# Performance work log

Measured on AMD Instinct MI355X. Metric: run time of the kernel, lower is better.

## Reference

```python
import jax, jax.numpy as jnp
import numpy as np

H = 768
NH = 12
HD = 64
FF = 3072
EPS = 1e-12


def layer_norm(x, g, b):
    mu = jnp.mean(x, axis=-1, keepdims=True)
    var = jnp.mean((x - mu) ** 2, axis=-1, keepdims=True)
    return (x - mu) * jax.lax.rsqrt(var + EPS) * g + b


def setup_inputs() -> dict:
    key = jax.random.key(0)
    ks = jax.random.split(key, 16)
    B, S, L = 16, 512, 50
    s = 0.02
    return {
        "hidden_states": jax.random.normal(ks[0], (B, S, H), jnp.float32),
        "attention_mask": jnp.zeros((B, 1, 1, S), jnp.float32),
        "past_key": jax.random.normal(ks[1], (B, NH, L, HD), jnp.float32),
        "past_value": jax.random.normal(ks[2], (B, NH, L, HD), jnp.float32),
        "Wq": jax.random.normal(ks[3], (H, H), jnp.float32) * s,
        "bq": jnp.zeros((H,), jnp.float32),
        "Wk": jax.random.normal(ks[4], (H, H), jnp.float32) * s,
        "bk": jnp.zeros((H,), jnp.float32),
        "Wv": jax.random.normal(ks[5], (H, H), jnp.float32) * s,
        "bv": jnp.zeros((H,), jnp.float32),
        "Wo": jax.random.normal(ks[6], (H, H), jnp.float32) * s,
        "bo": jnp.zeros((H,), jnp.float32),
        "ln1_g": jnp.ones((H,), jnp.float32),
        "ln1_b": jnp.zeros((H,), jnp.float32),
        "Wi": jax.random.normal(ks[7], (H, FF), jnp.float32) * s,
        "bi": jnp.zeros((FF,), jnp.float32),
        "Wf": jax.random.normal(ks[8], (FF, H), jnp.float32) * s,
        "bf": jnp.zeros((H,), jnp.float32),
        "ln2_g": jnp.ones((H,), jnp.float32),
        "ln2_b": jnp.zeros((H,), jnp.float32),
    }


def reference(hidden_states, attention_mask, past_key, past_value,
              Wq, bq, Wk, bk, Wv, bv, Wo, bo, ln1_g, ln1_b,
              Wi, bi, Wf, bf, ln2_g, ln2_b):
    B, S, _ = hidden_states.shape
    L = past_key.shape[2]

    def heads(x):  # [B,S,H] -> [B,NH,S,HD]
        return x.reshape(B, S, NH, HD).transpose(0, 2, 1, 3)

    q = heads(hidden_states @ Wq + bq)
    k = heads(hidden_states @ Wk + bk)
    v = heads(hidden_states @ Wv + bv)

    # faithful to source bug: past_key_values[0] concatenated into BOTH k and v
    k = jnp.concatenate([past_key, k], axis=2)  # [B,NH,L+S,HD]
    v = jnp.concatenate([past_key, v], axis=2)

    scores = jnp.einsum('bhqd,bhkd->bhqk', q, k) / jnp.sqrt(jnp.float32(HD))
    # visual mask positions get +1.0 (torch.ones), faithful to source
    vis_mask = jnp.ones((B, 1, 1, L), scores.dtype)
    full_mask = jnp.concatenate([vis_mask, attention_mask], axis=-1)
    scores = scores + full_mask

    probs = jax.nn.softmax(scores, axis=-1)
    ctx = jnp.einsum('bhqk,bhkd->bhqd', probs, v)  # [B,NH,S,HD]
    ctx = ctx.transpose(0, 2, 1, 3).reshape(B, S, H)

    attn_out = layer_norm(ctx @ Wo + bo + hidden_states, ln1_g, ln1_b)

    inter = jax.nn.gelu(attn_out @ Wi + bi, approximate=False)
    layer_out = layer_norm(inter @ Wf + bf + attn_out, ln2_g, ln2_b)
    return layer_out
```

## Files before the change

### kernel.cpp

```cpp
#include <hip/hip_runtime.h>
#include <math.h>

#define HDIM 64
#define NHEAD 12
#define HDN 768
#define QKVN 2304
#define FFDIM 3072
#define LPAST 50
#define SEQ 512
#define NBATCH 16
#define TKV (LPAST + SEQ)
#define TKVP 576
#define MTOK (NBATCH * SEQ)
#define NBH (NBATCH * NHEAD)

typedef __attribute__((ext_vector_type(8))) short short8;
typedef __attribute__((ext_vector_type(4))) float f32x4;

__device__ __forceinline__ ushort f2bf(float x) {
    union { float f; unsigned u; } c; c.f = x;
    unsigned r = (c.u + 0x7fffu + ((c.u >> 16) & 1u)) >> 16;
    return (ushort)r;
}
__device__ __forceinline__ float bf2f(ushort u) { return __uint_as_float((unsigned)u << 16); }
__device__ __forceinline__ float geluf(float v) {
    return 0.5f * v * (1.0f + erff(v * 0.70710678118654752f));
}

#define GLOAD_LDS16(gsrc, ldst)                                                    \
    __builtin_amdgcn_global_load_lds(                                              \
        (const __attribute__((address_space(1))) void*)(gsrc),                     \
        (__attribute__((address_space(3))) void*)(ldst), 16, 0, 0)

__global__ __launch_bounds__(256) void cast_bf(const float* __restrict__ x,
                                               ushort* __restrict__ y, int n4) {
    int i = blockIdx.x * 256 + threadIdx.x;
    if (i >= n4) return;
    float4 v = ((const float4*)x)[i];
    ushort4 o; o.x = f2bf(v.x); o.y = f2bf(v.y); o.z = f2bf(v.z); o.w = f2bf(v.w);
    ((ushort4*)y)[i] = o;
}

__global__ __launch_bounds__(256) void pack_bias(const float* __restrict__ bq,
                                                 const float* __restrict__ bk,
                                                 const float* __restrict__ bv,
                                                 float* __restrict__ o) {
    int i = blockIdx.x * 256 + threadIdx.x;
    if (i >= QKVN) return;
    o[i] = i < HDN ? bq[i] : (i < 2 * HDN ? bk[i - HDN] : bv[i - 2 * HDN]);
}

__global__ __launch_bounds__(256) void transpose_cast(const float* __restrict__ W,
                                                      ushort* __restrict__ WT,
                                                      int K, int N) {
    __shared__ float t[32][33];
    const int n0 = blockIdx.x * 32, k0 = blockIdx.y * 32;
    const int tx = threadIdx.x & 31, ty = threadIdx.x >> 5;
    #pragma unroll
    for (int i = 0; i < 4; ++i)
        t[ty + i * 8][tx] = W[(size_t)(k0 + ty + i * 8) * N + n0 + tx];
    __syncthreads();
    #pragma unroll
    for (int i = 0; i < 4; ++i)
        WT[(size_t)(n0 + ty + i * 8) * K + k0 + tx] = f2bf(t[tx][ty + i * 8]);
}

__global__ __launch_bounds__(256) void transpose_cast4(
    const float* __restrict__ W0, const float* __restrict__ W1,
    const float* __restrict__ W2, const float* __restrict__ W3,
    ushort* __restrict__ T0, ushort* __restrict__ T1,
    ushort* __restrict__ T2, ushort* __restrict__ T3) {
    __shared__ float t[32][33];
    const int z = blockIdx.z;
    const float* W = z == 0 ? W0 : z == 1 ? W1 : z == 2 ? W2 : W3;
    ushort* WT = z == 0 ? T0 : z == 1 ? T1 : z == 2 ? T2 : T3;
    const int n0 = blockIdx.x * 32, k0 = blockIdx.y * 32;
    const int tx = threadIdx.x & 31, ty = threadIdx.x >> 5;
    #pragma unroll
    for (int i = 0; i < 4; ++i)
        t[ty + i * 8][tx] = W[(size_t)(k0 + ty + i * 8) * HDN + n0 + tx];
    __syncthreads();
    #pragma unroll
    for (int i = 0; i < 4; ++i)
        WT[(size_t)(n0 + ty + i * 8) * HDN + k0 + tx] = f2bf(t[tx][ty + i * 8]);
}

template<int EPI>
__global__ __launch_bounds__(256) void gemm_mfma3(
    const ushort* __restrict__ A, const ushort* __restrict__ B,
    int lda, int ldb,
    const float* __restrict__ bias, const float* __restrict__ resid,
    const ushort* __restrict__ resid_bf,
    void* __restrict__ Cout, int M, int N, int K)
{
    __shared__ ushort sm[3 * 8192];

    const int tid = threadIdx.x;
    const int lane = tid & 63;
    const int wv = tid >> 6;
    const int wr = wv >> 1, wc = wv & 1;
    const int bm = blockIdx.x * 128, bn = blockIdx.y * 128;
    const int lr = lane & 15, lg = lane >> 4;
    const int swzu = ((lr * 64 + lg * 16) ^ ((lr & 8) << 2)) >> 1;

    int srow[2], skk[2];
    #pragma unroll
    for (int r = 0; r < 2; ++r) {
        int o = (tid + 256 * r) * 16;
        int st = o >> 10;
        int q = o & 1023;
        q ^= ((q >> 9) & 1) << 5;
        srow[r] = st * 16 + (q >> 6);
        skk[r] = (q & 63) >> 1;
    }
    const ushort* Abase = A + (size_t)bm * lda;
    const ushort* Bbase = B + (size_t)bn * ldb;
    const int nt = K >> 5;

    f32x4 acc[4][4] = {};

#define STAGE(T, BUF)                                                            \
    do {                                                                         \
        const int k0_ = (T) << 5;                                                \
        ushort* base_ = sm + (BUF) * 8192;                                       \
        _Pragma("unroll")                                                        \
        for (int r_ = 0; r_ < 2; ++r_) {                                         \
            int sl_ = tid + 256 * r_;                                            \
            GLOAD_LDS16(Abase + (size_t)srow[r_] * lda + k0_ + skk[r_],          \
                        (char*)base_ + sl_ * 16);                                \
        }                                                                        \
        _Pragma("unroll")                                                        \
        for (int r_ = 0; r_ < 2; ++r_) {                                         \
            int sl_ = tid + 256 * r_;                                            \
            GLOAD_LDS16(Bbase + (size_t)srow[r_] * ldb + k0_ + skk[r_],          \
                        (char*)(base_ + 4096) + sl_ * 16);                       \
        }                                                                        \
    } while (0)

    STAGE(0, 0);
    STAGE(1, 1);
    asm volatile("s_waitcnt vmcnt(4)" ::: "memory");
    __builtin_amdgcn_sched_barrier(0);
    __builtin_amdgcn_s_barrier();
    __builtin_amdgcn_sched_barrier(0);

    int buf = 0;
    for (int t = 0; t < nt; ++t) {
        if (t + 2 < nt) {
            int nbuf = buf + 2; if (nbuf >= 3) nbuf -= 3;
            STAGE(t + 2, nbuf);
        }
        const ushort* ab = sm + buf * 8192;
        short8 af[4], bfv[4];
        #pragma unroll
        for (int i = 0; i < 4; ++i) {
            af[i]  = *(const short8*)(ab + (wr * 4 + i) * 512 + swzu);
            bfv[i] = *(const short8*)(ab + 4096 + (wc * 4 + i) * 512 + swzu);
        }
        __builtin_amdgcn_s_setprio(1);
        #pragma unroll
        for (int i = 0; i < 4; ++i)
            #pragma unroll
            for (int j = 0; j < 4; ++j)
                acc[i][j] = __builtin_amdgcn_mfma_f32_16x16x32_bf16(
                    af[i], bfv[j], acc[i][j], 0, 0, 0);
        __builtin_amdgcn_s_setprio(0);
        if (t + 2 < nt)
            asm volatile("s_waitcnt vmcnt(4)" ::: "memory");
        else
            asm volatile("s_waitcnt vmcnt(0)" ::: "memory");
        __builtin_amdgcn_sched_barrier(0);
        __builtin_amdgcn_s_barrier();
        __builtin_amdgcn_sched_barrier(0);
        buf = buf + 1 == 3 ? 0 : buf + 1;
    }
#undef STAGE

    #pragma unroll
    for (int i = 0; i < 4; ++i) {
        #pragma unroll
        for (int j = 0; j < 4; ++j) {
            const int col = bn + wc * 64 + j * 16 + lr;
            const float bv = bias[col];
            #pragma unroll
            for (int rr = 0; rr < 4; ++rr) {
                const int row = bm + wr * 64 + i * 16 + (lane >> 4) * 4 + rr;
                const size_t idx = (size_t)row * N + col;
                float v = acc[i][j][rr] + bv;
                if (EPI == 0) {
                    ((ushort*)Cout)[idx] = f2bf(v);
                } else if (EPI == 1) {
                    ((float*)Cout)[idx] = v + resid[idx];
                } else if (EPI == 2) {
                    ((ushort*)Cout)[idx] = f2bf(geluf(v));
                } else {
                    ((float*)Cout)[idx] = v + bf2f(resid_bf[idx]);
                }
            }
        }
    }
}

__global__ __launch_bounds__(256) void kvK(
    const ushort* __restrict__ qkv, const float* __restrict__ past_key,
    ushort* __restrict__ kf)
{
    const size_t total = (size_t)NBH * TKV * HDIM;
    size_t idx = (size_t)blockIdx.x * 256 + threadIdx.x;
    if (idx >= total) return;
    int d = idx & 63;
    size_t r = idx >> 6;
    int t = (int)(r % TKV);
    int bh = (int)(r / TKV);
    ushort kv_;
    if (t < LPAST) {
        kv_ = f2bf(past_key[((size_t)bh * LPAST + t) * HDIM + d]);
    } else {
        int b = bh / NHEAD, h = bh % NHEAD;
        kv_ = qkv[((size_t)(b * SEQ + (t - LPAST))) * QKVN + HDN + h * HDIM + d];
    }
    kf[idx] = kv_;
}

__global__ __launch_bounds__(256) void kvVT(
    const ushort* __restrict__ qkv, const float* __restrict__ past_key,
    ushort* __restrict__ vt)
{
    __shared__ ushort td[64][72];
    const int bh = blockIdx.x / 9;
    const int t0 = (blockIdx.x % 9) * 64;
    const int b = bh / NHEAD, h = bh % NHEAD;
    const int trow = threadIdx.x >> 2, seg = threadIdx.x & 3;
    const int t = t0 + trow;

    ushort vals[16];
    if (t < LPAST) {
        const float* pk = past_key + ((size_t)bh * LPAST + t) * HDIM + seg * 16;
        #pragma unroll
        for (int i = 0; i < 4; ++i) {
            float4 f = ((const float4*)pk)[i];
            vals[i * 4 + 0] = f2bf(f.x); vals[i * 4 + 1] = f2bf(f.y);
            vals[i * 4 + 2] = f2bf(f.z); vals[i * 4 + 3] = f2bf(f.w);
        }
    } else if (t < TKV) {
        const ushort* vp = qkv + ((size_t)(b * SEQ + (t - LPAST))) * QKVN
                               + 2 * HDN + h * HDIM + seg * 16;
        uint4 u0 = ((const uint4*)vp)[0], u1 = ((const uint4*)vp)[1];
        *(uint4*)&vals[0] = u0; *(uint4*)&vals[8] = u1;
    } else {
        #pragma unroll
        for (int i = 0; i < 16; ++i) vals[i] = 0;
    }
    #pragma unroll
    for (int i = 0; i < 16; ++i) td[trow][seg * 16 + i] = vals[i];
    __syncthreads();

    const int d = threadIdx.x >> 2;
    ushort o[16];
    #pragma unroll
    for (int i = 0; i < 16; ++i) o[i] = td[seg * 16 + i][d];
    ushort* dst = vt + ((size_t)bh * HDIM + d) * TKVP + t0 + seg * 16;
    *(uint4*)dst = *(uint4*)&o[0];
    *(uint4*)(dst + 8) = *(uint4*)&o[8];
}

__global__ __launch_bounds__(256) void attn3(
    const ushort* __restrict__ qkv, const ushort* __restrict__ kf,
    const ushort* __restrict__ vt, const float* __restrict__ mask,
    ushort* __restrict__ ctx)
{
    __shared__ ushort Ks[64 * 64];
    __shared__ ushort Vs[64 * 64];
    __shared__ ushort Ps[4][16 * 64];

    const int wv = threadIdx.x >> 6, lane = threadIdx.x & 63;
    const int lr = lane & 15, lg = lane >> 4;
    const int bid = blockIdx.x;
    const int xcd = bid & 7, gi = bid >> 3;
    const int bh = xcd * (NBH / 8) + (gi >> 3);
    const int s0 = (gi & 7) * 64;
    const int b = bh / NHEAD, h = bh % NHEAD;

    short8 af[2];
    {
        const ushort* qp = qkv + ((size_t)(b * SEQ + s0 + wv * 16 + lr)) * QKVN
                               + h * HDIM + lg * 8;
        af[0] = *(const short8*)qp;
        af[1] = *(const short8*)(qp + 32);
    }

    const ushort* kbase = kf + (size_t)bh * TKV * HDIM;
    const ushort* vbase = vt + (size_t)bh * HDIM * TKVP;

    float m[4] = {-1e30f, -1e30f, -1e30f, -1e30f};
    float l[4] = {};
    f32x4 ctxa[4] = {};

    for (int kt = 0; kt < 9; ++kt) {
        const int t0 = kt * 64;
        #pragma unroll
        for (int r = 0; r < 2; ++r) {
            int sl = (int)threadIdx.x + 256 * r;
            int row = sl >> 3, p = sl & 7;
            int j = p ^ (row & 7);
            int trow = t0 + row; if (trow > TKV - 1) trow = TKV - 1;
            GLOAD_LDS16(kbase + ((size_t)trow << 6) + j * 8, (char*)Ks + sl * 16);
        }
        #pragma unroll
        for (int r = 0; r < 2; ++r) {
            int sl = (int)threadIdx.x + 256 * r;
            int row = sl >> 3, p = sl & 7;
            int j = p ^ (row & 7);
            GLOAD_LDS16(vbase + (size_t)row * TKVP + t0 + j * 8, (char*)Vs + sl * 16);
        }
        __syncthreads();

        f32x4 sa[4] = {};
        #pragma unroll
        for (int kb = 0; kb < 4; ++kb) {
            const int key = kb * 16 + lr;
            #pragma unroll
            for (int c = 0; c < 2; ++c) {
                const int phys = (c * 4 + lg) ^ (key & 7);
                short8 kfrag = *(const short8*)&Ks[key * 64 + phys * 8];
                sa[kb] = __builtin_amdgcn_mfma_f32_16x16x32_bf16(
                    af[c], kfrag, sa[kb], 0, 0, 0);
            }
        }

        float scv[4][4];
        #pragma unroll
        for (int kb = 0; kb < 4; ++kb) {
            const int t = t0 + kb * 16 + lr;
            float add = 0.0f;
            bool dead = (t >= TKV);
            if (!dead) add = (t < LPAST) ? 1.0f : mask[(size_t)b * SEQ + (t - LPAST)];
            #pragma unroll
            for (int r = 0; r < 4; ++r)
                scv[kb][r] = dead ? -1e30f : fmaf(sa[kb][r], 0.125f, add);
        }

        #pragma unroll
        for (int r = 0; r < 4; ++r) {
            float mx = fmaxf(fmaxf(scv[0][r], scv[1][r]), fmaxf(scv[2][r], scv[3][r]));
            mx = fmaxf(mx, __shfl_xor(mx, 1));
            mx = fmaxf(mx, __shfl_xor(mx, 2));
            mx = fmaxf(mx, __shfl_xor(mx, 4));
            mx = fmaxf(mx, __shfl_xor(mx, 8));
            const float mn = fmaxf(m[r], mx);
            const float f = __expf(m[r] - mn);
            m[r] = mn;
            l[r] *= f;
            #pragma unroll
            for (int dg = 0; dg < 4; ++dg) ctxa[dg][r] *= f;
            const int q_ = lg * 4 + r;
            #pragma unroll
            for (int kb = 0; kb < 4; ++kb) {
                float p = __expf(scv[kb][r] - mn);
                l[r] += p;
                const int key = kb * 16 + lr;
                const int phys = (key >> 3) ^ (q_ & 7);
                Ps[wv][q_ * 64 + phys * 8 + (key & 7)] = f2bf(p);
            }
        }

        short8 pa[2];
        #pragma unroll
        for (int c = 0; c < 2; ++c) {
            const int phys = (c * 4 + lg) ^ (lr & 7);
            pa[c] = *(const short8*)&Ps[wv][lr * 64 + phys * 8];
        }
        #pragma unroll
        for (int dg = 0; dg < 4; ++dg) {
            const int d = dg * 16 + lr;
            #pragma unroll
            for (int c = 0; c < 2; ++c) {
                const int phys = (c * 4 + lg) ^ (d & 7);
                short8 vfrag = *(const short8*)&Vs[d * 64 + phys * 8];
                ctxa[dg] = __builtin_amdgcn_mfma_f32_16x16x32_bf16(
                    pa[c], vfrag, ctxa[dg], 0, 0, 0);
            }
        }
        __syncthreads();
    }

    #pragma unroll
    for (int r = 0; r < 4; ++r) {
        float s = l[r];
        s += __shfl_xor(s, 1); s += __shfl_xor(s, 2);
        s += __shfl_xor(s, 4); s += __shfl_xor(s, 8);
        l[r] = 1.0f / s;
    }
    #pragma unroll
    for (int r = 0; r < 4; ++r) {
        const int q_ = s0 + wv * 16 + lg * 4 + r;
        const size_t base = ((size_t)(b * SEQ + q_)) * HDN + h * HDIM;
        #pragma unroll
        for (int dg = 0; dg < 4; ++dg)
            ctx[base + dg * 16 + lr] = f2bf(ctxa[dg][r] * l[r]);
    }
}

__global__ __launch_bounds__(256) void layernorm2(
    const float* __restrict__ x, const float* __restrict__ g,
    const float* __restrict__ b, float* __restrict__ out,
    ushort* __restrict__ out_bf)
{
    const size_t row = blockIdx.x;
    const float* xr = &x[row * HDN];
    const int t = threadIdx.x;

    float v0 = xr[t], v1 = xr[t + 256], v2 = xr[t + 512];

    __shared__ float red[4];
    float s = v0 + v1 + v2;
    #pragma unroll
    for (int off = 32; off > 0; off >>= 1) s += __shfl_xor(s, off);
    if ((t & 63) == 0) red[t >> 6] = s;
    __syncthreads();
    float mean = (red[0] + red[1] + red[2] + red[3]) * (1.0f / 768.0f);

    float d0 = v0 - mean, d1 = v1 - mean, d2 = v2 - mean;
    float vs = d0 * d0 + d1 * d1 + d2 * d2;
    #pragma unroll
    for (int off = 32; off > 0; off >>= 1) vs += __shfl_xor(vs, off);
    __syncthreads();
    if ((t & 63) == 0) red[t >> 6] = vs;
    __syncthreads();
    float var = (red[0] + red[1] + red[2] + red[3]) * (1.0f / 768.0f);
    float rstd = rsqrtf(var + 1e-12f);

    float o0 = d0 * rstd * g[t] + b[t];
    float o1 = d1 * rstd * g[t + 256] + b[t + 256];
    float o2 = d2 * rstd * g[t + 512] + b[t + 512];
    if (out) {
        out[row * HDN + t] = o0;
        out[row * HDN + t + 256] = o1;
        out[row * HDN + t + 512] = o2;
    }
    if (out_bf) {
        out_bf[row * HDN + t] = f2bf(o0);
        out_bf[row * HDN + t + 256] = f2bf(o1);
        out_bf[row * HDN + t + 512] = f2bf(o2);
    }
}

extern "C" void kernel_launch(void* const* d_in, const int* in_sizes, int n_in,
                              void* d_out, int out_size, void* d_ws, size_t ws_size,
                              hipStream_t stream) {
    const float* hs       = (const float*)d_in[0];
    const float* mask     = (const float*)d_in[1];
    const float* past_key = (const float*)d_in[2];
    const float* Wq = (const float*)d_in[4];
    const float* bq = (const float*)d_in[5];
    const float* Wk = (const float*)d_in[6];
    const float* bk = (const float*)d_in[7];
    const float* Wv = (const float*)d_in[8];
    const float* bv = (const float*)d_in[9];
    const float* Wo = (const float*)d_in[10];
    const float* bo = (const float*)d_in[11];
    const float* ln1_g = (const float*)d_in[12];
    const float* ln1_b = (const float*)d_in[13];
    const float* Wi = (const float*)d_in[14];
    const float* bi = (const float*)d_in[15];
    const float* Wf = (const float*)d_in[16];
    const float* bf_ = (const float*)d_in[17];
    const float* ln2_g = (const float*)d_in[18];
    const float* ln2_b = (const float*)d_in[19];
    float* out = (float*)d_out;

    char* w = (char*)d_ws;
    ushort* WqT   = (ushort*)(w + 0);
    ushort* WoT   = (ushort*)(w + 3538944);
    ushort* WiT   = (ushort*)(w + 4718592);
    ushort* WfT   = (ushort*)(w + 9437184);
    float*  bqkv  = (float*)(w + 14155776);
    ushort* hs_bf = (ushort*)(w + 14172160);
    ushort* qkv   = (ushort*)(w + 26755072);
    ushort* kf    = (ushort*)(w + 64503808);
    ushort* vt    = (ushort*)(w + 78315520);
    ushort* ctx_bf = hs_bf;
    float*  tmp   = (float*)(w + 64503808);
    ushort* inter = (ushort*)(w + 14172160);
    ushort* aln_bf = (ushort*)(w + 89669632);
    ushort* WkT = WqT + (size_t)HDN * HDN;
    ushort* WvT = WqT + (size_t)2 * HDN * HDN;

    dim3 b256(256);

    cast_bf<<<dim3((MTOK * HDN / 4 + 255) / 256), b256, 0, stream>>>(hs, hs_bf, MTOK * HDN / 4);
    pack_bias<<<dim3(9), b256, 0, stream>>>(bq, bk, bv, bqkv);
    transpose_cast4<<<dim3(24, 24, 4), b256, 0, stream>>>(Wq, Wk, Wv, Wo, WqT, WkT, WvT, WoT);
    transpose_cast<<<dim3(96, 24), b256, 0, stream>>>(Wi, WiT, HDN, FFDIM);
    transpose_cast<<<dim3(24, 96), b256, 0, stream>>>(Wf, WfT, FFDIM, HDN);

    gemm_mfma3<0><<<dim3(MTOK / 128, QKVN / 128), b256, 0, stream>>>(
        hs_bf, WqT, HDN, HDN, bqkv, nullptr, nullptr, qkv, MTOK, QKVN, HDN);

    {
        size_t ktot = (size_t)NBH * TKV * HDIM;
        kvK<<<dim3((unsigned)((ktot + 255) / 256)), b256, 0, stream>>>(qkv, past_key, kf);
    }
    kvVT<<<dim3(NBH * 9), b256, 0, stream>>>(qkv, past_key, vt);

    attn3<<<dim3(NBH * 8), b256, 0, stream>>>(qkv, kf, vt, mask, ctx_bf);

    gemm_mfma3<1><<<dim3(MTOK / 128, HDN / 128), b256, 0, stream>>>(
        ctx_bf, WoT, HDN, HDN, bo, hs, nullptr, tmp, MTOK, HDN, HDN);
    layernorm2<<<dim3(MTOK), b256, 0, stream>>>(tmp, ln1_g, ln1_b, nullptr, aln_bf);

    gemm_mfma3<2><<<dim3(MTOK / 128, FFDIM / 128), b256, 0, stream>>>(
        aln_bf, WiT, HDN, HDN, bi, nullptr, nullptr, inter, MTOK, FFDIM, HDN);
    gemm_mfma3<4><<<dim3(MTOK / 128, HDN / 128), b256, 0, stream>>>(
        inter, WfT, FFDIM, FFDIM, bf_, nullptr, aln_bf, tmp, MTOK, HDN, FFDIM);

    layernorm2<<<dim3(MTOK), b256, 0, stream>>>(tmp, ln2_g, ln2_b, out, nullptr);
}
```

Baseline: 275.1 us.

## Add 256x256-tile 8-wave GEMM with 128KB LDS for QKV and FFN-up projections

Adds a new bf16 MFMA GEMM kernel that uses 256x256 output tiles, 512 threads (8 waves), double-buffered 128KB dynamic LDS with XOR swizzling, and interleaved LDS reads, global prefetches and MFMA phases with priority hints. It replaces the 128x128 kernel for the QKV projection and the GELU intermediate GEMM. The aim is higher arithmetic intensity and less global/LDS traffic per FLOP. In exchange it runs one block per CU, and the grids shrink to 32x9 and 32x12 blocks, which may underfill a 256-CU device.

```diff
diff --git a/kernel.cpp b/kernel.cpp
--- a/kernel.cpp
+++ b/kernel.cpp
@@ -83,6 +83,166 @@
     #pragma unroll
     for (int i = 0; i < 4; ++i)
         WT[(size_t)(n0 + ty + i * 8) * HDN + k0 + tx] = f2bf(t[tx][ty + i * 8]);
+}
+
+template<int EPI>
+__global__ __launch_bounds__(512, 1) void gemm8(
+    const ushort* __restrict__ A, const ushort* __restrict__ B,
+    int lda, int ldb, const float* __restrict__ bias,
+    ushort* __restrict__ Cout, int M, int N, int K)
+{
+    extern __shared__ ushort sm[];
+
+    const int tid = threadIdx.x;
+    const int lane = tid & 63;
+    const int wv = tid >> 6;
+    const int wm = wv >> 2, wn = wv & 3;
+    const int lr = lane & 15, lg = lane >> 4;
+    const int bm = blockIdx.x * 256, bn = blockIdx.y * 256;
+    const int nt = K >> 6;
+
+    int srow[2], scol[2];
+    #pragma unroll
+    for (int r = 0; r < 2; ++r) {
+        int o = (tid + 512 * r) * 16;
+        int row = o >> 7;
+        int c16 = (o >> 4) & 7;
+        srow[r] = row;
+        scol[r] = (c16 ^ (row & 7)) * 8;
+    }
+
+#define STG8(srcbase, ld, dstb)                                              \
+    _Pragma("unroll")                                                        \
+    for (int r_ = 0; r_ < 2; ++r_)                                           \
+        GLOAD_LDS16((srcbase) + (size_t)srow[r_] * (ld) + scol[r_],          \
+                    (char*)sm + (dstb) + (tid + 512 * r_) * 16);
+
+#define STGB(T)                                                              \
+    do { int bb_ = ((T) & 1) * 65536 + 32768;                                \
+        STG8(B + (size_t)bn * ldb + (size_t)(T) * 64, ldb, bb_);             \
+        STG8(B + (size_t)(bn + 128) * ldb + (size_t)(T) * 64, ldb, bb_ + 16384); } while (0)
+#define STGA(T)                                                              \
+    do { int ab_ = ((T) & 1) * 65536;                                        \
+        STG8(A + (size_t)bm * lda + (size_t)(T) * 64, lda, ab_);             \
+        STG8(A + (size_t)(bm + 128) * lda + (size_t)(T) * 64, lda, ab_ + 16384); } while (0)
+
+    STGB(0); STGA(0);
+    STGB(1); STGA(1);
+    asm volatile("s_waitcnt vmcnt(8)" ::: "memory");
+    __builtin_amdgcn_sched_barrier(0);
+    __builtin_amdgcn_s_barrier();
+    __builtin_amdgcn_sched_barrier(0);
+
+    const int swz0 = (lg * 8) ^ ((lr & 7) << 3);
+    const int swz1 = (32 + lg * 8) ^ ((lr & 7) << 3);
+
+    short8 af[4][2], bq[4][2];
+    f32x4 acc[8][4] = {};
+
+    for (int T = 0; T < nt; ++T) {
+        const ushort* Ab = sm + (T & 1) * 32768 + wm * 8192;
+        const ushort* Bb = sm + (T & 1) * 32768 + 16384 + (wn >> 1) * 8192 + (wn & 1) * 4096;
+
+        #pragma unroll
+        for (int m = 0; m < 4; ++m) {
+            af[m][0] = *(const short8*)(Ab + (m * 16 + lr) * 64 + swz0);
+            af[m][1] = *(const short8*)(Ab + (m * 16 + lr) * 64 + swz1);
+        }
+        #pragma unroll
+        for (int n = 0; n < 2; ++n) {
+            bq[n][0] = *(const short8*)(Bb + (n * 16 + lr) * 64 + swz0);
+            bq[n][1] = *(const short8*)(Bb + (n * 16 + lr) * 64 + swz1);
+        }
+        __builtin_amdgcn_s_barrier();
+        asm volatile("s_waitcnt lgkmcnt(0)" ::: "memory");
+        __builtin_amdgcn_sched_barrier(0);
+        __builtin_amdgcn_s_setprio(1);
+        #pragma unroll
+        for (int m = 0; m < 4; ++m)
+            #pragma unroll
+            for (int n = 0; n < 2; ++n) {
+                acc[m][n] = __builtin_amdgcn_mfma_f32_16x16x32_bf16(af[m][0], bq[n][0], acc[m][n], 0, 0, 0);
+                acc[m][n] = __builtin_amdgcn_mfma_f32_16x16x32_bf16(af[m][1], bq[n][1], acc[m][n], 0, 0, 0);
+            }
+        __builtin_amdgcn_s_setprio(0);
+
+        #pragma unroll
+        for (int n = 2; n < 4; ++n) {
+            bq[n][0] = *(const short8*)(Bb + (n * 16 + lr) * 64 + swz0);
+            bq[n][1] = *(const short8*)(Bb + (n * 16 + lr) * 64 + swz1);
+        }
+        __builtin_amdgcn_s_barrier();
+        asm volatile("s_waitcnt lgkmcnt(0)" ::: "memory");
+        __builtin_amdgcn_sched_barrier(0);
+        __builtin_amdgcn_s_setprio(1);
+        #pragma unroll
+        for (int m = 0; m < 4; ++m)
+            #pragma unroll
+            for (int n = 2; n < 4; ++n) {
+                acc[m][n] = __builtin_amdgcn_mfma_f32_16x16x32_bf16(af[m][0], bq[n][0], acc[m][n], 0, 0, 0);
+                acc[m][n] = __builtin_amdgcn_mfma_f32_16x16x32_bf16(af[m][1], bq[n][1], acc[m][n], 0, 0, 0);
+            }
+        __builtin_amdgcn_s_setprio(0);
+
+        #pragma unroll
+        for (int m = 0; m < 4; ++m) {
+            af[m][0] = *(const short8*)(Ab + ((m + 4) * 16 + lr) * 64 + swz0);
+            af[m][1] = *(const short8*)(Ab + ((m + 4) * 16 + lr) * 64 + swz1);
+        }
+        __builtin_amdgcn_s_barrier();
+        if (T + 2 < nt) { STGB(T + 2); }
+        asm volatile("s_waitcnt lgkmcnt(0)" ::: "memory");
+        __builtin_amdgcn_sched_barrier(0);
+        __builtin_amdgcn_s_setprio(1);
+        #pragma unroll
+        for (int m = 0; m < 4; ++m)
+            #pragma unroll
+            for (int n = 0; n < 2; ++n) {
+                acc[m + 4][n] = __builtin_amdgcn_mfma_f32_16x16x32_bf16(af[m][0], bq[n][0], acc[m + 4][n], 0, 0, 0);
+                acc[m + 4][n] = __builtin_amdgcn_mfma_f32_16x16x32_bf16(af[m][1], bq[n][1], acc[m + 4][n], 0, 0, 0);
+            }
+        __builtin_amdgcn_s_setprio(0);
+
+        __builtin_amdgcn_s_barrier();
+        if (T + 2 < nt) { STGA(T + 2); }
+        __builtin_amdgcn_sched_barrier(0);
+        __builtin_amdgcn_s_setprio(1);
+        #pragma unroll
+        for (int m = 0; m < 4; ++m)
+            #pragma unroll
+            for (int n = 2; n < 4; ++n) {
+                acc[m + 4][n] = __builtin_amdgcn_mfma_f32_16x16x32_bf16(af[m][0], bq[n][0], acc[m + 4][n], 0, 0, 0);
+                acc[m + 4][n] = __builtin_amdgcn_mfma_f32_16x16x32_bf16(af[m][1], bq[n][1], acc[m + 4][n], 0, 0, 0);
+            }
+        __builtin_amdgcn_s_setprio(0);
+
+        if (T < nt - 1) {
+            if (T + 2 < nt) asm volatile("s_waitcnt vmcnt(8)" ::: "memory");
+            else            asm volatile("s_waitcnt vmcnt(0)" ::: "memory");
+            __builtin_amdgcn_sched_barrier(0);
+            __builtin_amdgcn_s_barrier();
+            __builtin_amdgcn_sched_barrier(0);
+        }
+    }
+#undef STGA
+#undef STGB
+#undef STG8
+
+    #pragma unroll
+    for (int m = 0; m < 8; ++m) {
+        #pragma unroll
+        for (int n = 0; n < 4; ++n) {
+            const int col = bn + wn * 64 + n * 16 + lr;
+            const float bv = bias[col];
+            #pragma unroll
+            for (int rr = 0; rr < 4; ++rr) {
+                const int row = bm + wm * 128 + m * 16 + lg * 4 + rr;
+                const size_t idx = (size_t)row * N + col;
+                float v = acc[m][n][rr] + bv;
+                Cout[idx] = f2bf(EPI == 2 ? geluf(v) : v);
+            }
+        }
+    }
 }
 
 template<int EPI>
@@ -184,15 +344,11 @@
             const float bv = bias[col];
             #pragma unroll
             for (int rr = 0; rr < 4; ++rr) {
-                const int row = bm + wr * 64 + i * 16 + (lane >> 4) * 4 + rr;
+                const int row = bm + wr * 64 + i * 16 + lg * 4 + rr;
                 const size_t idx = (size_t)row * N + col;
                 float v = acc[i][j][rr] + bv;
-                if (EPI == 0) {
-                    ((ushort*)Cout)[idx] = f2bf(v);
-                } else if (EPI == 1) {
+                if (EPI == 1) {
                     ((float*)Cout)[idx] = v + resid[idx];
-                } else if (EPI == 2) {
-                    ((ushort*)Cout)[idx] = f2bf(geluf(v));
                 } else {
                     ((float*)Cout)[idx] = v + bf2f(resid_bf[idx]);
                 }
@@ -488,14 +644,19 @@
 
     dim3 b256(256);
 
+    hipFuncSetAttribute((const void*)&gemm8<0>,
+                        hipFuncAttributeMaxDynamicSharedMemorySize, 131072);
+    hipFuncSetAttribute((const void*)&gemm8<2>,
+                        hipFuncAttributeMaxDynamicSharedMemorySize, 131072);
+
     cast_bf<<<dim3((MTOK * HDN / 4 + 255) / 256), b256, 0, stream>>>(hs, hs_bf, MTOK * HDN / 4);
     pack_bias<<<dim3(9), b256, 0, stream>>>(bq, bk, bv, bqkv);
     transpose_cast4<<<dim3(24, 24, 4), b256, 0, stream>>>(Wq, Wk, Wv, Wo, WqT, WkT, WvT, WoT);
     transpose_cast<<<dim3(96, 24), b256, 0, stream>>>(Wi, WiT, HDN, FFDIM);
     transpose_cast<<<dim3(24, 96), b256, 0, stream>>>(Wf, WfT, FFDIM, HDN);
 
-    gemm_mfma3<0><<<dim3(MTOK / 128, QKVN / 128), b256, 0, stream>>>(
-        hs_bf, WqT, HDN, HDN, bqkv, nullptr, nullptr, qkv, MTOK, QKVN, HDN);
+    gemm8<0><<<dim3(MTOK / 256, QKVN / 256), dim3(512), 131072, stream>>>(
+        hs_bf, WqT, HDN, HDN, bqkv, qkv, MTOK, QKVN, HDN);
 
     {
         size_t ktot = (size_t)NBH * TKV * HDIM;
@@ -509,8 +670,8 @@
         ctx_bf, WoT, HDN, HDN, bo, hs, nullptr, tmp, MTOK, HDN, HDN);
     layernorm2<<<dim3(MTOK), b256, 0, stream>>>(tmp, ln1_g, ln1_b, nullptr, aln_bf);
 
-    gemm_mfma3<2><<<dim3(MTOK / 128, FFDIM / 128), b256, 0, stream>>>(
-        aln_bf, WiT, HDN, HDN, bi, nullptr, nullptr, inter, MTOK, FFDIM, HDN);
+    gemm8<2><<<dim3(MTOK / 256, FFDIM / 256), dim3(512), 131072, stream>>>(
+        aln_bf, WiT, HDN, HDN, bi, inter, MTOK, FFDIM, HDN);
     gemm_mfma3<4><<<dim3(MTOK / 128, HDN / 128), b256, 0, stream>>>(
         inter, WfT, FFDIM, FFDIM, bf_, nullptr, aln_bf, tmp, MTOK, HDN, FFDIM);
 
```

Result: slower. 298.0 us (+8.3%).
